# Performance work log

Hardware: AMD Instinct MI355X
Metric: run time of the kernel (lower is better)

## Reference

```python
import jax, jax.numpy as jnp
import numpy as np

NUM_ATOMS = 100
D = 32        # initial_atom_dim
H = 16        # hidden_dim (multiplicity per irrep)
NB = 16       # edge_dim / number of bessel basis functions
CUT = 6.0     # radius_cutoff
DEG = 4.0     # degree_norm
OUT = 1       # output_dim
INV4PI = 1.0 / np.sqrt(4.0 * np.pi)  # 'integral' SH normalization


def _bessel(d, nb, cut):
    # e3nn soft_one_hot_linspace(basis='bessel', cutoff=True) * sqrt(nb)
    x = d[:, None]
    n = jnp.arange(1, nb + 1, dtype=d.dtype)
    safe = jnp.maximum(x, 1e-9)
    out = np.sqrt(2.0 / cut) * jnp.sin(n * jnp.pi * x / cut) / safe
    return out * (x < cut) * np.sqrt(float(nb))


def _fc(x, w1, w2):
    # e3nn FullyConnectedNet: fan-in normalized linear layers, silu, no bias
    h = jax.nn.silu(x @ w1 / np.sqrt(x.shape[-1]))
    return h @ w2 / np.sqrt(w1.shape[-1])


def _forward(atomic_numbers, edge_index, coords, atom_emb,
             fc0_w1, fc0_w2, fc1_w1, fc1_w2, w_readout):
    src, dst = edge_index[0], edge_index[1]
    N = coords.shape[0]
    E = src.shape[0]

    vec = coords[src] - coords[dst]                      # [E,3]
    dist = jnp.linalg.norm(vec, axis=-1)                 # [E]
    unit = vec / jnp.maximum(dist, 1e-9)[:, None]

    # spherical harmonics, l=0 and l=1, 'integral' normalization
    y0 = jnp.full((E,), INV4PI, dtype=coords.dtype)      # [E]
    y1 = (np.sqrt(3.0) * INV4PI) * unit                  # [E,3]
    basis = _bessel(dist, NB, CUT)                       # [E,NB]

    x = atom_emb[atomic_numbers]                         # [N,D] (row 0 is padding)

    # ---- layer 0: scalars (D x0e) x (1x0e+1x1o) -> H x0e + H x1o ----
    w = _fc(basis, fc0_w1, fc0_w2)                       # [E, 2*D*H] per-edge TP weights
    wa = w[:, : D * H].reshape(E, D, H)
    wb = w[:, D * H:].reshape(E, D, H)
    xs = x[src]
    n0 = 1.0 / np.sqrt(D)                                # path fan-in norm
    m0 = jnp.einsum('ed,edh->eh', xs, wa) * y0[:, None] * n0          # [E,H]
    m1 = jnp.einsum('ed,edh->eh', xs, wb)[:, :, None] * y1[:, None, :] * n0  # [E,H,3]
    z0 = jax.ops.segment_sum(m0, dst, num_segments=N) / DEG           # [N,H]
    z1 = jax.ops.segment_sum(m1, dst, num_segments=N) / DEG           # [N,H,3]

    # ---- layer 1: (H x0e + H x1o) x (1x0e+1x1o) -> same irreps, skip-connected ----
    w = _fc(basis, fc1_w1, fc1_w2)                       # [E, 4*H*H]
    w1_ = w[:, 0 * H * H:1 * H * H].reshape(E, H, H)     # 0e x 0e -> 0e
    w2_ = w[:, 1 * H * H:2 * H * H].reshape(E, H, H)     # 0e x 1o -> 1o
    w3_ = w[:, 2 * H * H:3 * H * H].reshape(E, H, H)     # 1o x 0e -> 1o
    w4_ = w[:, 3 * H * H:4 * H * H].reshape(E, H, H)     # 1o x 1o -> 0e (CG = dot/sqrt(3))
    s, v = z0[src], z1[src]
    n1 = 1.0 / np.sqrt(2 * H)                            # two paths per output irrep
    dot = jnp.einsum('ehm,em->eh', v, y1) / np.sqrt(3.0)
    o0 = (jnp.einsum('eh,ehk->ek', s, w1_) * y0[:, None]
          + jnp.einsum('eh,ehk->ek', dot, w4_)) * n1
    o1 = (jnp.einsum('eh,ehk->ek', s, w2_)[:, :, None] * y1[:, None, :]
          + jnp.einsum('ehm,ehk->ekm', v, w3_) * y0[:, None, None]) * n1
    z0 = jax.ops.segment_sum(o0, dst, num_segments=N) / DEG + z0      # skip
    z1 = jax.ops.segment_sum(o1, dst, num_segments=N) / DEG + z1

    # ---- scalar readout (o3.Linear onto 0e) + graph sum-pool ----
    node_scalar = z0 @ w_readout / np.sqrt(H)            # [N,OUT]
    return jnp.sum(node_scalar, axis=0)                  # [OUT]


def setup_inputs() -> dict:
    key = jax.random.key(0)
    ks = jax.random.split(key, 9)
    N, E = 10000, 160000
    atomic_numbers = jax.random.randint(ks[0], (N,), 0, NUM_ATOMS)
    coords = jax.random.normal(ks[1], (N, 3), dtype=jnp.float32)
    edge_index = jax.random.randint(ks[2], (2, E), 0, N)
    atom_emb = jax.random.normal(ks[3], (NUM_ATOMS, D), dtype=jnp.float32).at[0].set(0.0)
    fc0_w1 = jax.random.normal(ks[4], (NB, H), dtype=jnp.float32)
    fc0_w2 = jax.random.normal(ks[5], (H, 2 * D * H), dtype=jnp.float32)
    fc1_w1 = jax.random.normal(ks[6], (NB, H), dtype=jnp.float32)
    fc1_w2 = jax.random.normal(ks[7], (H, 4 * H * H), dtype=jnp.float32)
    w_readout = jax.random.normal(ks[8], (H, OUT), dtype=jnp.float32)
    return {"atomic_numbers": atomic_numbers, "coords": coords, "edge_index": edge_index,
            "atom_emb": atom_emb, "fc0_w1": fc0_w1, "fc0_w2": fc0_w2,
            "fc1_w1": fc1_w1, "fc1_w2": fc1_w2, "w_readout": w_readout}


def reference(atomic_numbers, coords, edge_index, atom_emb,
              fc0_w1, fc0_w2, fc1_w1, fc1_w2, w_readout):
    return _forward(atomic_numbers, edge_index, coords, atom_emb,
                    fc0_w1, fc0_w2, fc1_w1, fc1_w2, w_readout)
```

## Files before the change

### kernel.cpp

```cpp
#include <hip/hip_runtime.h>
#include <math.h>


namespace {
constexpr int   NATOMS   = 100;
constexpr int   CAP      = 64;
constexpr float PI_F     = 3.14159265358979323846f;
constexpr float INV4PI_F = 0.28209479177387814f;
constexpr float SQRT3_F  = 1.7320508075688772f;
constexpr float CUT_F    = 6.0f;
constexpr float BASIS_C  = 2.3094010767585034f;
constexpr float N0_F     = 0.17677669529663687f;
constexpr float K0_F = INV4PI_F * N0_F * 0.0625f;
constexpr float K1_F = SQRT3_F * INV4PI_F * N0_F * 0.0625f;
}

__device__ __forceinline__ float silu_fast(float x) {
  return x / (1.0f + __expf(-x));
}

__device__ __forceinline__ float block_reduce_sum(float v) {
  #pragma unroll
  for (int o = 32; o > 0; o >>= 1) v += __shfl_down(v, o, 64);
  __shared__ float ls[8];
  int lane = threadIdx.x & 63;
  int w    = threadIdx.x >> 6;
  if (lane == 0) ls[w] = v;
  __syncthreads();
  float s = 0.f;
  if (threadIdx.x == 0) {
    int nw = (blockDim.x + 63) >> 6;
    for (int i = 0; i < nw; ++i) s += ls[i];
  }
  return s;
}

__global__ void setup_kernel(const float* __restrict__ atom_emb,
                             const float* __restrict__ fc0_w2,
                             const float* __restrict__ fc1_w2,
                             const float* __restrict__ w_readout,
                             const int* __restrict__ ei,
                             float* __restrict__ T0, float* __restrict__ T1,
                             float* __restrict__ G1T, float* __restrict__ G4T,
                             int* __restrict__ cursor, int* __restrict__ elist,
                             int E) {
  int b = blockIdx.x;
  int tt = threadIdx.x;
  if (b < NATOMS) {
    int j = tt >> 4;
    int h = tt & 15;
    float s0 = 0.f, s1 = 0.f;
    #pragma unroll
    for (int d = 0; d < 32; ++d) {
      float x = atom_emb[b * 32 + d];
      s0 = fmaf(x, fc0_w2[j * 1024 + d * 16 + h], s0);
      s1 = fmaf(x, fc0_w2[j * 1024 + 512 + d * 16 + h], s1);
    }
    T0[b * 256 + tt] = s0;
    T1[b * 256 + tt] = s1;
  } else if (b == NATOMS) {
    int j = tt >> 4;
    int h = tt & 15;
    float g1 = 0.f, g4 = 0.f;
    #pragma unroll
    for (int k = 0; k < 16; ++k) {
      float r = w_readout[k];
      g1 = fmaf(fc1_w2[j * 1024 + h * 16 + k], r, g1);
      g4 = fmaf(fc1_w2[j * 1024 + 768 + h * 16 + k], r, g4);
    }
    G1T[h * 16 + j] = g1;
    G4T[h * 16 + j] = g4;
  } else {
    int e = (b - NATOMS - 1) * blockDim.x + tt;
    if (e < E) {
      int d = ei[E + e];
      int pos = atomicAdd(&cursor[d], 1);
      if (pos < CAP) elist[d * CAP + pos] = ei[e];
    }
  }
}

__global__ void __launch_bounds__(256, 4)
gather_kernel(const int* __restrict__ elist,
              const int* __restrict__ cursor,
              const float* __restrict__ coords,
              const int* __restrict__ an,
              const float* __restrict__ fc0_w1,
              const float* __restrict__ T0,
              const float* __restrict__ T1,
              const float* __restrict__ G1T,
              const float* __restrict__ G4T,
              const float* __restrict__ w_readout,
              float* __restrict__ zbuf,
              float* __restrict__ out,
              int N) {
  __shared__ float ggs[512];
  ggs[threadIdx.x]       = G1T[threadIdx.x];
  ggs[256 + threadIdx.x] = G4T[threadIdx.x];
  __syncthreads();

  int wave = threadIdx.x >> 6;
  int lane = threadIdx.x & 63;
  int g    = lane >> 4;
  int t    = lane & 15;
  int base = lane & 48;
  int node = blockIdx.x * 4 + wave;
  bool valid = node < N;

  float w0c[16];
  #pragma unroll
  for (int k = 0; k < 16; ++k) w0c[k] = fc0_w1[k * 16 + t];
  float rr = w_readout[t];

  float cnx = 0.f, cny = 0.f, cnz = 0.f;
  int cnt = 0;
  if (valid) {
    cnx = coords[3 * node + 0];
    cny = coords[3 * node + 1];
    cnz = coords[3 * node + 2];
    cnt = min(cursor[node], CAP);
  }
  const int* eb = elist + (size_t)(valid ? node : 0) * CAP;

  const float angc = PI_F / CUT_F;
  float acc0 = 0.f, accx = 0.f, accy = 0.f, accz = 0.f;

  for (int i = g; i < cnt; i += 8) {
    int iB = i + 4;
    bool hasB = iB < cnt;
    int sA = eb[i];
    int sB = hasB ? eb[iB] : sA;

    float pxA = coords[3 * sA + 0], pyA = coords[3 * sA + 1], pzA = coords[3 * sA + 2];
    float pxB = coords[3 * sB + 0], pyB = coords[3 * sB + 1], pzB = coords[3 * sB + 2];
    int aA = an[sA], aB = an[sB];

    float vxA = pxA - cnx, vyA = pyA - cny, vzA = pzA - cnz;
    float vxB = pxB - cnx, vyB = pyB - cny, vzB = pzB - cnz;
    float dA = sqrtf(vxA * vxA + vyA * vyA + vzA * vzA);
    float dB = sqrtf(vxB * vxB + vyB * vyB + vzB * vzB);
    float ivA = 1.0f / fmaxf(dA, 1e-9f);
    float ivB = 1.0f / fmaxf(dB, 1e-9f);
    float uxA = vxA * ivA, uyA = vyA * ivA, uzA = vzA * ivA;
    float uxB = vxB * ivB, uyB = vyB * ivB, uzB = vzB * ivB;
    float bcA = (dA < CUT_F) ? (BASIS_C * ivA) : 0.0f;
    float bcB = (dB < CUT_F) ? (BASIS_C * ivB) : 0.0f;

    float angA = angc * dA, angB = angc * dB;
    float scA = __sinf(angA), twA = 2.0f * __cosf(angA), spA = 0.f, hA = 0.f;
    float scB = __sinf(angB), twB = 2.0f * __cosf(angB), spB = 0.f, hB = 0.f;
    #pragma unroll
    for (int k = 0; k < 16; ++k) {
      hA = fmaf(scA, w0c[k], hA);
      hB = fmaf(scB, w0c[k], hB);
      float snA = fmaf(twA, scA, -spA); spA = scA; scA = snA;
      float snB = fmaf(twB, scB, -spB); spB = scB; scB = snB;
    }
    float h0A = silu_fast(hA * bcA * 0.25f);
    float h0B = silu_fast(hB * bcB * 0.25f);

    const float* t0A = T0 + aA * 256 + t;
    const float* t1A = T1 + aA * 256 + t;
    const float* t0B = T0 + aB * 256 + t;
    const float* t1B = T1 + aB * 256 + t;
    float u0A = 0.f, u1A = 0.f, u0B = 0.f, u1B = 0.f;
    #pragma unroll
    for (int j = 0; j < 16; ++j) {
      float hjA = __shfl(h0A, base + j, 64);
      float hjB = __shfl(h0B, base + j, 64);
      u0A = fmaf(hjA, t0A[j * 16], u0A);
      u1A = fmaf(hjA, t1A[j * 16], u1A);
      u0B = fmaf(hjB, t0B[j * 16], u0B);
      u1B = fmaf(hjB, t1B[j * 16], u1B);
    }
    float mB = hasB ? 1.0f : 0.0f;
    acc0 += u0A + mB * u0B;
    accx = fmaf(u1A, uxA, fmaf(mB * u1B, uxB, accx));
    accy = fmaf(u1A, uyA, fmaf(mB * u1B, uyB, accy));
    accz = fmaf(u1A, uzA, fmaf(mB * u1B, uzB, accz));
  }

  acc0 += __shfl_xor(acc0, 16, 64); acc0 += __shfl_xor(acc0, 32, 64);
  accx += __shfl_xor(accx, 16, 64); accx += __shfl_xor(accx, 32, 64);
  accy += __shfl_xor(accy, 16, 64); accy += __shfl_xor(accy, 32, 64);
  accz += __shfl_xor(accz, 16, 64); accz += __shfl_xor(accz, 32, 64);

  float srcv = (g == 0) ? acc0 * K0_F
                        : ((g == 1) ? accx : (g == 2) ? accy : accz) * K1_F;
  int tofs = (g == 0) ? 0 : 256;
  float o = 0.f;
  #pragma unroll
  for (int h = 0; h < 16; ++h) {
    float vh = __shfl(srcv, base + h, 64);
    o = fmaf(ggs[tofs + h * 16 + t], vh, o);
  }
  if (valid) zbuf[(size_t)node * 64 + t * 4 + g] = o;

  float p = (valid && g == 0) ? acc0 * K0_F * rr : 0.f;
  float tot = block_reduce_sum(p);
  if (threadIdx.x == 0) atomicAdd(out, tot * 0.25f);
}

__global__ void __launch_bounds__(256, 4)
phase2_kernel(const int* __restrict__ ei,
              const float* __restrict__ coords,
              const float* __restrict__ fc1_w1,
              const float* __restrict__ zbuf,
              float* __restrict__ out,
              int E) {
  int t = threadIdx.x & 15;
  float w1c[16];
  #pragma unroll
  for (int k = 0; k < 16; ++k) w1c[k] = fc1_w1[k * 16 + t];

  int gid = (blockIdx.x * blockDim.x + threadIdx.x) >> 4;
  int ngroups = (gridDim.x * blockDim.x) >> 4;
  const float angc = PI_F / CUT_F;

  float c = 0.f;
  for (int e = gid; e < E; e += ngroups) {
    int s = ei[e];
    int d = ei[E + e];
    float vx = coords[3 * s + 0] - coords[3 * d + 0];
    float vy = coords[3 * s + 1] - coords[3 * d + 1];
    float vz = coords[3 * s + 2] - coords[3 * d + 2];
    float dist = sqrtf(vx * vx + vy * vy + vz * vz);
    float inv  = 1.0f / fmaxf(dist, 1e-9f);
    float ux = vx * inv, uy = vy * inv, uz = vz * inv;
    float bc = (dist < CUT_F) ? (BASIS_C * inv) : 0.0f;

    float ang = angc * dist;
    float sc = __sinf(ang);
    float tw = 2.0f * __cosf(ang);
    float sp = 0.f, acc = 0.f;
    #pragma unroll
    for (int k = 0; k < 16; ++k) {
      acc = fmaf(sc, w1c[k], acc);
      float sn = fmaf(tw, sc, -sp);
      sp = sc; sc = sn;
    }
    float h1t = silu_fast(acc * bc * 0.25f);

    float4 z = ((const float4*)(zbuf + (size_t)s * 64))[t];
    c = fmaf(h1t, fmaf(z.y, ux, fmaf(z.z, uy, fmaf(z.w, uz, z.x))), c);
  }
  c *= INV4PI_F * N0_F * (1.0f / 64.0f);
  float tot = block_reduce_sum(c);
  if (threadIdx.x == 0) atomicAdd(out, tot);
}

extern "C" void kernel_launch(void* const* d_in, const int* in_sizes, int n_in,
                              void* d_out, int out_size, void* d_ws, size_t ws_size,
                              hipStream_t stream) {
  const int*   an        = (const int*)d_in[0];
  const float* coords    = (const float*)d_in[1];
  const int*   ei        = (const int*)d_in[2];
  const float* atom_emb  = (const float*)d_in[3];
  const float* fc0_w1    = (const float*)d_in[4];
  const float* fc0_w2    = (const float*)d_in[5];
  const float* fc1_w1    = (const float*)d_in[6];
  const float* fc1_w2    = (const float*)d_in[7];
  const float* w_readout = (const float*)d_in[8];

  int N = in_sizes[0];
  int E = in_sizes[2] / 2;

  float* ws   = (float*)d_ws;
  float* zbuf = ws;
  float* T0   = zbuf + (size_t)N * 64;
  float* T1   = T0 + NATOMS * 256;
  float* G1T  = T1 + NATOMS * 256;
  float* G4T  = G1T + 256;
  int*   cursor = (int*)(G4T + 256);
  int*   elist  = cursor + N;
  float* out = (float*)d_out;

  hipMemsetAsync(cursor, 0, (size_t)N * sizeof(int), stream);
  hipMemsetAsync(out, 0, sizeof(float), stream);

  int blk = 256;
  int ebkts = (E + blk - 1) / blk;
  setup_kernel<<<NATOMS + 1 + ebkts, blk, 0, stream>>>(
      atom_emb, fc0_w2, fc1_w2, w_readout, ei,
      T0, T1, G1T, G4T, cursor, elist, E);

  gather_kernel<<<(N + 3) / 4, blk, 0, stream>>>(
      elist, cursor, coords, an, fc0_w1, T0, T1, G1T, G4T, w_readout,
      zbuf, out, N);

  phase2_kernel<<<2048, blk, 0, stream>>>(ei, coords, fc1_w1, zbuf, out, E);
}
```

Baseline: 165.0 us.

## Interleave T0/T1 tables and run gather as one wave per node

Interleaves the per-atom T0 and T1 tables into a single TI array so each lane reads one float2 per j instead of two scalar loads. The gather kernel switches from 256-thread blocks with four nodes each to 64-thread blocks with one node each. Readout weights now live in per-lane registers instead of shared memory, which removes the LDS staging and its __syncthreads. The block reduction becomes a wave shuffle reduction, at the cost of one atomicAdd per node instead of one per four nodes, plus more registers.

Result: slower. 254.9 us (+54.5%).

```diff
diff --git a/kernel.cpp b/kernel.cpp
--- a/kernel.cpp
+++ b/kernel.cpp
@@ -40,7 +40,7 @@
                              const float* __restrict__ fc1_w2,
                              const float* __restrict__ w_readout,
                              const int* __restrict__ ei,
-                             float* __restrict__ T0, float* __restrict__ T1,
+                             float* __restrict__ TI,
                              float* __restrict__ G1T, float* __restrict__ G4T,
                              int* __restrict__ cursor, int* __restrict__ elist,
                              int E) {
@@ -56,8 +56,8 @@
       s0 = fmaf(x, fc0_w2[j * 1024 + d * 16 + h], s0);
       s1 = fmaf(x, fc0_w2[j * 1024 + 512 + d * 16 + h], s1);
     }
-    T0[b * 256 + tt] = s0;
-    T1[b * 256 + tt] = s1;
+    TI[b * 512 + j * 32 + 2 * h]     = s0;
+    TI[b * 512 + j * 32 + 2 * h + 1] = s1;
   } else if (b == NATOMS) {
     int j = tt >> 4;
     int h = tt & 15;
@@ -80,47 +80,39 @@
   }
 }
 
-__global__ void __launch_bounds__(256, 4)
+__global__ void __launch_bounds__(64)
 gather_kernel(const int* __restrict__ elist,
               const int* __restrict__ cursor,
               const float* __restrict__ coords,
               const int* __restrict__ an,
               const float* __restrict__ fc0_w1,
-              const float* __restrict__ T0,
-              const float* __restrict__ T1,
+              const float* __restrict__ TI,
               const float* __restrict__ G1T,
               const float* __restrict__ G4T,
               const float* __restrict__ w_readout,
               float* __restrict__ zbuf,
               float* __restrict__ out,
               int N) {
-  __shared__ float ggs[512];
-  ggs[threadIdx.x]       = G1T[threadIdx.x];
-  ggs[256 + threadIdx.x] = G4T[threadIdx.x];
-  __syncthreads();
-
-  int wave = threadIdx.x >> 6;
-  int lane = threadIdx.x & 63;
+  int lane = threadIdx.x;
   int g    = lane >> 4;
   int t    = lane & 15;
   int base = lane & 48;
-  int node = blockIdx.x * 4 + wave;
-  bool valid = node < N;
-
-  float w0c[16];
-  #pragma unroll
-  for (int k = 0; k < 16; ++k) w0c[k] = fc0_w1[k * 16 + t];
+  int node = blockIdx.x;
+
+  float w0c[16], gcol[16];
+  const float* gp = (g == 0) ? G1T : G4T;
+  #pragma unroll
+  for (int k = 0; k < 16; ++k) {
+    w0c[k]  = fc0_w1[k * 16 + t];
+    gcol[k] = gp[k * 16 + t];
+  }
   float rr = w_readout[t];
 
-  float cnx = 0.f, cny = 0.f, cnz = 0.f;
-  int cnt = 0;
-  if (valid) {
-    cnx = coords[3 * node + 0];
-    cny = coords[3 * node + 1];
-    cnz = coords[3 * node + 2];
-    cnt = min(cursor[node], CAP);
-  }
-  const int* eb = elist + (size_t)(valid ? node : 0) * CAP;
+  float cnx = coords[3 * node + 0];
+  float cny = coords[3 * node + 1];
+  float cnz = coords[3 * node + 2];
+  int cnt = min(cursor[node], CAP);
+  const int* eb = elist + (size_t)node * CAP;
 
   const float angc = PI_F / CUT_F;
   float acc0 = 0.f, accx = 0.f, accy = 0.f, accz = 0.f;
@@ -147,31 +139,31 @@
     float bcB = (dB < CUT_F) ? (BASIS_C * ivB) : 0.0f;
 
     float angA = angc * dA, angB = angc * dB;
-    float scA = __sinf(angA), twA = 2.0f * __cosf(angA), spA = 0.f, hA = 0.f;
-    float scB = __sinf(angB), twB = 2.0f * __cosf(angB), spB = 0.f, hB = 0.f;
+    float scA = __sinf(angA), twA = 2.0f * __cosf(angA), spA = 0.f, hAa = 0.f;
+    float scB = __sinf(angB), twB = 2.0f * __cosf(angB), spB = 0.f, hBa = 0.f;
     #pragma unroll
     for (int k = 0; k < 16; ++k) {
-      hA = fmaf(scA, w0c[k], hA);
-      hB = fmaf(scB, w0c[k], hB);
+      hAa = fmaf(scA, w0c[k], hAa);
+      hBa = fmaf(scB, w0c[k], hBa);
       float snA = fmaf(twA, scA, -spA); spA = scA; scA = snA;
       float snB = fmaf(twB, scB, -spB); spB = scB; scB = snB;
     }
-    float h0A = silu_fast(hA * bcA * 0.25f);
-    float h0B = silu_fast(hB * bcB * 0.25f);
-
-    const float* t0A = T0 + aA * 256 + t;
-    const float* t1A = T1 + aA * 256 + t;
-    const float* t0B = T0 + aB * 256 + t;
-    const float* t1B = T1 + aB * 256 + t;
+    float h0A = silu_fast(hAa * bcA * 0.25f);
+    float h0B = silu_fast(hBa * bcB * 0.25f);
+
+    const float2* tpA = (const float2*)(TI + aA * 512) + t;
+    const float2* tpB = (const float2*)(TI + aB * 512) + t;
     float u0A = 0.f, u1A = 0.f, u0B = 0.f, u1B = 0.f;
     #pragma unroll
     for (int j = 0; j < 16; ++j) {
       float hjA = __shfl(h0A, base + j, 64);
       float hjB = __shfl(h0B, base + j, 64);
-      u0A = fmaf(hjA, t0A[j * 16], u0A);
-      u1A = fmaf(hjA, t1A[j * 16], u1A);
-      u0B = fmaf(hjB, t0B[j * 16], u0B);
-      u1B = fmaf(hjB, t1B[j * 16], u1B);
+      float2 TA = tpA[j * 16];
+      float2 TB = tpB[j * 16];
+      u0A = fmaf(hjA, TA.x, u0A);
+      u1A = fmaf(hjA, TA.y, u1A);
+      u0B = fmaf(hjB, TB.x, u0B);
+      u1B = fmaf(hjB, TB.y, u1B);
     }
     float mB = hasB ? 1.0f : 0.0f;
     acc0 += u0A + mB * u0B;
@@ -187,18 +179,18 @@
 
   float srcv = (g == 0) ? acc0 * K0_F
                         : ((g == 1) ? accx : (g == 2) ? accy : accz) * K1_F;
-  int tofs = (g == 0) ? 0 : 256;
   float o = 0.f;
   #pragma unroll
   for (int h = 0; h < 16; ++h) {
     float vh = __shfl(srcv, base + h, 64);
-    o = fmaf(ggs[tofs + h * 16 + t], vh, o);
-  }
-  if (valid) zbuf[(size_t)node * 64 + t * 4 + g] = o;
-
-  float p = (valid && g == 0) ? acc0 * K0_F * rr : 0.f;
-  float tot = block_reduce_sum(p);
-  if (threadIdx.x == 0) atomicAdd(out, tot * 0.25f);
+    o = fmaf(gcol[h], vh, o);
+  }
+  zbuf[(size_t)node * 64 + t * 4 + g] = o;
+
+  float p = (g == 0) ? acc0 * K0_F * rr : 0.f;
+  #pragma unroll
+  for (int o2 = 8; o2 > 0; o2 >>= 1) p += __shfl_down(p, o2, 64);
+  if (lane == 0) atomicAdd(out, p * 0.25f);
 }
 
 __global__ void __launch_bounds__(256, 4)
@@ -267,9 +259,8 @@
 
   float* ws   = (float*)d_ws;
   float* zbuf = ws;
-  float* T0   = zbuf + (size_t)N * 64;
-  float* T1   = T0 + NATOMS * 256;
-  float* G1T  = T1 + NATOMS * 256;
+  float* TI   = zbuf + (size_t)N * 64;
+  float* G1T  = TI + NATOMS * 512;
   float* G4T  = G1T + 256;
   int*   cursor = (int*)(G4T + 256);
   int*   elist  = cursor + N;
@@ -282,10 +273,10 @@
   int ebkts = (E + blk - 1) / blk;
   setup_kernel<<<NATOMS + 1 + ebkts, blk, 0, stream>>>(
       atom_emb, fc0_w2, fc1_w2, w_readout, ei,
-      T0, T1, G1T, G4T, cursor, elist, E);
-
-  gather_kernel<<<(N + 3) / 4, blk, 0, stream>>>(
-      elist, cursor, coords, an, fc0_w1, T0, T1, G1T, G4T, w_readout,
+      TI, G1T, G4T, cursor, elist, E);
+
+  gather_kernel<<<N, 64, 0, stream>>>(
+      elist, cursor, coords, an, fc0_w1, TI, G1T, G4T, w_readout,
       zbuf, out, N);
 
   phase2_kernel<<<2048, blk, 0, stream>>>(ei, coords, fc1_w1, zbuf, out, E);
```
